# Performance work log

Measured on AMD Instinct MI355X. Metric: run time of the kernel, lower is better.

Reference implementation:

```python
import jax, jax.numpy as jnp
import numpy as np
from jax import lax

D_MODEL = 512
D_INNER = 1024   # expand=2
D_STATE = 16
D_CONV = 4
DT_RANK = 32     # ceil(d_model/16)
D_FFN = 2048
EPS = 1e-6


def _layernorm(x, g, b):
    mu = jnp.mean(x, axis=-1, keepdims=True)
    var = jnp.mean((x - mu) ** 2, axis=-1, keepdims=True)
    return (x - mu) * lax.rsqrt(var + EPS) * g + b


def _mamba(x, in_w, conv_w, conv_b, xproj_w, dt_w, dt_b, A_log, D_vec, out_w):
    # x: [B, L, d_model]
    B, L, _ = x.shape
    xz = jnp.einsum('bld,ed->ble', x, in_w)           # [B, L, 2*d_inner]
    xc, z = xz[..., :D_INNER], xz[..., D_INNER:]
    # causal depthwise conv over time
    xt = xc.transpose(0, 2, 1)                        # [B, d_inner, L]
    kern = conv_w[:, None, :]                         # [d_inner, 1, d_conv]
    xt = lax.conv_general_dilated(xt, kern, (1,), [(D_CONV - 1, 0)],
                                  feature_group_count=D_INNER)
    xc = jax.nn.silu(xt.transpose(0, 2, 1) + conv_b)  # [B, L, d_inner]
    # input-dependent SSM parameters
    x_dbl = jnp.einsum('bld,ed->ble', xc, xproj_w)    # [B, L, dt_rank+2*d_state]
    dt = x_dbl[..., :DT_RANK]
    Bm = x_dbl[..., DT_RANK:DT_RANK + D_STATE]
    Cm = x_dbl[..., DT_RANK + D_STATE:]
    delta = jax.nn.softplus(jnp.einsum('blr,dr->bld', dt, dt_w) + dt_b)  # [B, L, d_inner]
    A = -jnp.exp(A_log)                               # [d_inner, d_state]

    def step(h, inp):
        d_t, u_t, b_t, c_t = inp                      # [B,di],[B,di],[B,ds],[B,ds]
        dA = jnp.exp(d_t[:, :, None] * A)             # [B, di, ds]
        dBu = (d_t * u_t)[:, :, None] * b_t[:, None, :]
        h = dA * h + dBu
        y = jnp.einsum('bds,bs->bd', h, c_t)
        return h, y

    h0 = jnp.zeros((B, D_INNER, D_STATE), x.dtype)
    xs = (delta.transpose(1, 0, 2), xc.transpose(1, 0, 2),
          Bm.transpose(1, 0, 2), Cm.transpose(1, 0, 2))
    _, ys = lax.scan(step, h0, xs)                    # [L, B, d_inner]
    y = ys.transpose(1, 0, 2) + xc * D_vec
    y = y * jax.nn.silu(z)
    return jnp.einsum('ble,de->bld', y, out_w)        # [B, L, d_model]


def setup_inputs() -> dict:
    key = jax.random.key(0)
    ks = iter(jax.random.split(key, 40))
    B, S, T = 8, 512, 1024

    def nrm(shape, scale=0.02):
        return jax.random.normal(next(ks), shape, dtype=jnp.float32) * scale

    def mamba_params(prefix):
        A_log = jnp.log(jnp.broadcast_to(jnp.arange(1, D_STATE + 1, dtype=jnp.float32),
                                         (D_INNER, D_STATE)))
        return {
            prefix + '_in_w': nrm((2 * D_INNER, D_MODEL)),
            prefix + '_conv_w': nrm((D_INNER, D_CONV), 0.1),
            prefix + '_conv_b': jnp.zeros((D_INNER,), jnp.float32),
            prefix + '_xproj_w': nrm((DT_RANK + 2 * D_STATE, D_INNER)),
            prefix + '_dt_w': nrm((D_INNER, DT_RANK), 0.1),
            prefix + '_dt_b': jnp.full((D_INNER,), -4.0, jnp.float32),
            prefix + '_A_log': A_log,
            prefix + '_D_vec': jnp.ones((D_INNER,), jnp.float32),
            prefix + '_out_w': nrm((D_MODEL, D_INNER)),
        }

    inp = {
        'tgt': jax.random.normal(next(ks), (B, S, D_MODEL), dtype=jnp.float32),
        'memory': jax.random.normal(next(ks), (B, T, D_MODEL), dtype=jnp.float32),
    }
    inp.update(mamba_params('self'))
    inp.update(mamba_params('cross'))
    inp.update({
        'ln1_g': jnp.ones((D_MODEL,), jnp.float32), 'ln1_b': jnp.zeros((D_MODEL,), jnp.float32),
        'ln2_g': jnp.ones((D_MODEL,), jnp.float32), 'ln2_b': jnp.zeros((D_MODEL,), jnp.float32),
        'ln3_g': jnp.ones((D_MODEL,), jnp.float32), 'ln3_b': jnp.zeros((D_MODEL,), jnp.float32),
        'ffn_w1': nrm((D_FFN, D_MODEL)), 'ffn_b1': jnp.zeros((D_FFN,), jnp.float32),
        'ffn_w2': nrm((D_MODEL, D_FFN)), 'ffn_b2': jnp.zeros((D_MODEL,), jnp.float32),
    })
    return inp


def reference(tgt, memory,
              self_in_w, self_conv_w, self_conv_b, self_xproj_w, self_dt_w, self_dt_b,
              self_A_log, self_D_vec, self_out_w,
              cross_in_w, cross_conv_w, cross_conv_b, cross_xproj_w, cross_dt_w, cross_dt_b,
              cross_A_log, cross_D_vec, cross_out_w,
              ln1_g, ln1_b, ln2_g, ln2_b, ln3_g, ln3_b,
              ffn_w1, ffn_b1, ffn_w2, ffn_b2):
    S = tgt.shape[1]
    # self-Mamba block (post-norm, dropout=0)
    t2 = _mamba(tgt, self_in_w, self_conv_w, self_conv_b, self_xproj_w,
                self_dt_w, self_dt_b, self_A_log, self_D_vec, self_out_w)
    t = _layernorm(tgt + t2, ln1_g, ln1_b)
    # cross-Mamba: scan over [memory; tgt], keep last S steps
    cat = jnp.concatenate([memory, t], axis=1)
    c2 = _mamba(cat, cross_in_w, cross_conv_w, cross_conv_b, cross_xproj_w,
                cross_dt_w, cross_dt_b, cross_A_log, cross_D_vec, cross_out_w)[:, -S:]
    t = _layernorm(t + c2, ln2_g, ln2_b)
    # positionwise FFN
    f = jnp.einsum('bld,fd->blf', t, ffn_w1) + ffn_b1
    f = jax.nn.relu(f)
    f = jnp.einsum('blf,df->bld', f, ffn_w2) + ffn_b2
    t = _layernorm(t + f, ln3_g, ln3_b)
    return t
```

## Files before the change

kernel.cpp:

```cpp
#include <hip/hip_runtime.h>
#include <math.h>

#define DM    512
#define DI    1024
#define DSN   16
#define DTR   32
#define DFFN  2048
#define BB    8
#define SS    512
#define TTM   1024
#define LCAT  1536
#define NC    64
#define CONV_R 8

#define ACT_NONE     0
#define ACT_RELU     1
#define ACT_DELTA    3
#define ACT_XDBL     4

typedef __attribute__((ext_vector_type(8))) short short8;
typedef __attribute__((ext_vector_type(8))) unsigned short ushort8;
typedef __attribute__((ext_vector_type(4))) float f32x4;

#define L2E 1.4426950408889634f

__device__ __forceinline__ unsigned short f2b(float f) {
    unsigned int u = __float_as_uint(f);
    return (unsigned short)((u + 0x7FFFu + ((u >> 16) & 1u)) >> 16);
}
__device__ __forceinline__ float b2f(unsigned short h) {
    return __uint_as_float(((unsigned int)h) << 16);
}
__device__ __forceinline__ float fast_softplus(float v) {
    return (v > 20.f) ? v : __logf(1.f + __expf(v));
}
__device__ __forceinline__ float fexp2(float x) {
#if __has_builtin(__builtin_amdgcn_exp2f)
    return __builtin_amdgcn_exp2f(x);
#else
    float r; asm("v_exp_f32 %0, %1" : "=v"(r) : "v"(x)); return r;
#endif
}
__device__ __forceinline__ float frcp(float x) {
    return __builtin_amdgcn_rcpf(x);
}
__device__ __forceinline__ void gld16(const void* g, void* l) {
    __builtin_amdgcn_global_load_lds(
        (const __attribute__((address_space(1))) void*)g,
        (__attribute__((address_space(3))) void*)l, 16, 0, 0);
}

__device__ __forceinline__ int map_row(int m, int mb, int bs, int ro) {
    int q = m / mb;
    return q * bs + ro + (m - q * mb);
}

__global__ __launch_bounds__(256) void mgemm_kernel(
    const unsigned short* __restrict__ A, int mb, int bs, int ro,
    const unsigned short* __restrict__ W, const float* __restrict__ bias,
    float* __restrict__ Cf, unsigned short* __restrict__ Cb,
    float* __restrict__ C2, float* __restrict__ Cf2,
    int N, int K, int act,
    int omb, int obs, int oro, int ldc, int nofs)
{
    __shared__ __align__(16) unsigned short As[128 * 64];
    __shared__ __align__(16) unsigned short Bs[128 * 64];
    int tid = threadIdx.x;
    int lane = tid & 63, wave = tid >> 6;
    int wy = wave >> 1, wx = wave & 1;
    int nx = gridDim.x;
    int f = blockIdx.y * nx + blockIdx.x;
    int xcd = f & 7, j2 = f >> 3;
    int bandh = gridDim.y >> 3;
    int m0 = (xcd * bandh + j2 / nx) * 128;
    int n0 = (j2 % nx) * 128;
    int Kh = K / gridDim.z;
    int kbeg = blockIdx.z * Kh, kend = kbeg + Kh;
    float* Cfo = Cf;
    const float* biaso = bias;
    if (blockIdx.z) { Cfo = Cf2; biaso = nullptr; }

    const unsigned short* ga[4];
    const unsigned short* gb[4];
    unsigned short* la[4];
    unsigned short* lb[4];
    #pragma unroll
    for (int j = 0; j < 4; j++) {
        int c  = wave * 256 + j * 64 + lane;
        int r  = c >> 3;
        int q  = c & 7;
        int g  = (q & 4) | ((q & 3) ^ (r & 3));
        int arow = map_row(m0 + r, mb, bs, ro);
        ga[j] = A + (size_t)arow * K + g * 8;
        gb[j] = W + (size_t)(n0 + r) * K + g * 8;
        la[j] = As + (size_t)(wave * 256 + j * 64) * 8;
        lb[j] = Bs + (size_t)(wave * 256 + j * 64) * 8;
    }
    int fm = lane & 15, fg = lane >> 4;
    int sw = fg ^ (fm & 3);
    const unsigned short* arp = As + ((size_t)(wy * 64 + fm) * 8 + sw) * 8;
    const unsigned short* brp = Bs + ((size_t)(wx * 64 + fm) * 8 + sw) * 8;

    f32x4 acc[4][4];
    #pragma unroll
    for (int i = 0; i < 4; i++)
        #pragma unroll
        for (int j = 0; j < 4; j++) acc[i][j] = 0.f;

    for (int k0 = kbeg; k0 < kend; k0 += 64) {
        #pragma unroll
        for (int j = 0; j < 4; j++) {
            gld16(ga[j] + k0, la[j]);
            gld16(gb[j] + k0, lb[j]);
        }
        __syncthreads();
        #pragma unroll
        for (int h = 0; h < 2; h++) {
            short8 af[4], bfr[4];
            #pragma unroll
            for (int t = 0; t < 4; t++) af[t]  = *(const short8*)(arp + h * 32 + t * 1024);
            #pragma unroll
            for (int t = 0; t < 4; t++) bfr[t] = *(const short8*)(brp + h * 32 + t * 1024);
            #pragma unroll
            for (int i = 0; i < 4; i++)
                #pragma unroll
                for (int j = 0; j < 4; j++)
                    acc[i][j] = __builtin_amdgcn_mfma_f32_16x16x32_bf16(af[i], bfr[j], acc[i][j], 0, 0, 0);
        }
        __syncthreads();
    }

    int en = lane & 15, em = (lane >> 4) * 4;
    if (act == ACT_XDBL) {
        #pragma unroll
        for (int j = 0; j < 4; j++) {
            int n = n0 + wx * 64 + j * 16 + en;
            if (n >= 64) continue;
            #pragma unroll
            for (int i = 0; i < 4; i++) {
                int mbase = m0 + wy * 64 + i * 16 + em;
                #pragma unroll
                for (int r = 0; r < 4; r++) {
                    float v = acc[i][j][r];
                    int m = mbase + r;
                    if (n < 32) {
                        Cb[(size_t)m * 64 + n] = f2b(v);
                    } else {
                        C2[(size_t)m * 32 + (n - 32)] = v;
                        Cb[(size_t)m * 64 + n] = 0;
                    }
                }
            }
        }
        return;
    }
    if (act == ACT_DELTA) {
        #pragma unroll
        for (int j = 0; j < 4; j++) {
            int n = n0 + wx * 64 + j * 16 + en;
            float bv = bias[n];
            #pragma unroll
            for (int i = 0; i < 4; i++) {
                int mbase = m0 + wy * 64 + i * 16 + em;
                #pragma unroll
                for (int r = 0; r < 4; r++) {
                    float v = acc[i][j][r] + bv;
                    Cb[(size_t)(mbase + r) * 1024 + n] = f2b(fast_softplus(v));
                }
            }
        }
        return;
    }
    #pragma unroll
    for (int j = 0; j < 4; j++) {
        int n = n0 + wx * 64 + j * 16 + en;
        float bv = biaso ? biaso[n] : 0.f;
        #pragma unroll
        for (int i = 0; i < 4; i++) {
            int mbase = m0 + wy * 64 + i * 16 + em;
            #pragma unroll
            for (int r = 0; r < 4; r++) {
                float v = acc[i][j][r] + bv;
                if (act == ACT_RELU) v = v > 0.f ? v : 0.f;
                int orow = map_row(mbase + r, omb, obs, oro);
                size_t off = (size_t)orow * ldc + nofs + n;
                if (Cb) Cb[off] = f2b(v);
                else    Cfo[off] = v;
            }
        }
    }
}

__global__ void xprojb_fill(const float* __restrict__ xproj, unsigned short* __restrict__ out)
{
    int idx = blockIdx.x * 256 + threadIdx.x;
    if (idx >= 131072) return;
    int n = idx >> 10;
    out[idx] = (n < 64) ? f2b(xproj[idx]) : (unsigned short)0;
}
__global__ void dtwb_fill(const float* __restrict__ dt_w, unsigned short* __restrict__ out)
{
    int idx = blockIdx.x * 256 + threadIdx.x;
    if (idx >= 65536) return;
    int n = idx >> 6, c = idx & 63;
    out[idx] = (c < 32) ? f2b(dt_w[n * 32 + c]) : (unsigned short)0;
}

__global__ __launch_bounds__(256) void conv_silu_kernel(
    const unsigned short* __restrict__ xz,
    const float* __restrict__ cw,
    const float* __restrict__ cb,
    unsigned short* __restrict__ xc, int L, int total)
{
    int idx = blockIdx.x * blockDim.x + threadIdx.x;
    if (idx >= total) return;
    int d8 = idx & 127;
    int d0 = d8 * 8;
    int t  = idx >> 7;
    int nq = L / CONV_R;
    int b  = t / nq;
    int l0 = (t - b * nq) * CONV_R;
    size_t rbase = (size_t)b * L + l0;

    float4 wv[8];
    #pragma unroll
    for (int j = 0; j < 8; j++) wv[j] = *(const float4*)(cw + (d0 + j) * 4);
    float bias[8];
    {
        float4 c0 = ((const float4*)(cb + d0))[0];
        float4 c1 = ((const float4*)(cb + d0))[1];
        bias[0]=c0.x; bias[1]=c0.y; bias[2]=c0.z; bias[3]=c0.w;
        bias[4]=c1.x; bias[5]=c1.y; bias[6]=c1.z; bias[7]=c1.w;
    }
    ushort8 win[CONV_R + 3];
    #pragma unroll
    for (int k = 0; k < 3; k++) {
        ushort8 z;
        #pragma unroll
        for (int j = 0; j < 8; j++) z[j] = 0;
        win[k] = (l0 - 3 + k >= 0)
            ? *(const ushort8*)(xz + (rbase - 3 + k) * 2048 + d0) : z;
    }
    #pragma unroll
    for (int i = 0; i < CONV_R; i++)
        win[3 + i] = *(const ushort8*)(xz + (rbase + i) * 2048 + d0);

    const float* w = (const float*)&wv[0];
    #pragma unroll
    for (int i = 0; i < CONV_R; i++) {
        float acc[8];
        #pragma unroll
        for (int j = 0; j < 8; j++) acc[j] = bias[j];
        #pragma unroll
        for (int k = 0; k < 4; k++) {
            ushort8 v = win[i + k];
            #pragma unroll
            for (int j = 0; j < 8; j++)
                acc[j] = fmaf(b2f(v[j]), w[j * 4 + k], acc[j]);
        }
        ushort8 o;
        #pragma unroll
        for (int j = 0; j < 8; j++)
            o[j] = f2b(acc[j] * frcp(1.f + __expf(-acc[j])));
        *(ushort8*)(xc + (rbase + i) * 1024 + d0) = o;
    }
}

__global__ __launch_bounds__(256) void scan_part1(
    const unsigned short* __restrict__ delta, const unsigned short* __restrict__ xc,
    const float* __restrict__ bc, const float* __restrict__ A_log,
    float* __restrict__ part_h, float* __restrict__ part_s, int L, int CH)
{
    int tid = threadIdx.x;
    int dblk = blockIdx.x & 3;
    int c    = (blockIdx.x >> 2) & (NC - 1);
    int b    = blockIdx.x / (4 * NC);
    int d    = dblk * 256 + tid;
    float A2[DSN];
    {
        const float4* ap = (const float4*)(A_log + d * DSN);
        #pragma unroll
        for (int q = 0; q < 4; q++) {
            float4 a4 = ap[q];
            A2[q*4+0] = -__expf(a4.x) * L2E;
            A2[q*4+1] = -__expf(a4.y) * L2E;
            A2[q*4+2] = -__expf(a4.z) * L2E;
            A2[q*4+3] = -__expf(a4.w) * L2E;
        }
    }
    float h[DSN];
    #pragma unroll
    for (int s = 0; s < DSN; s++) h[s] = 0.f;
    float ssum = 0.f;
    int l0 = c * CH;
    for (int l = l0; l < l0 + CH; l++) {
        size_t r = (size_t)b * L + l;
        float4 bq[4];
        const float4* bp = (const float4*)(bc + r * 32);
        #pragma unroll
        for (int q = 0; q < 4; q++) bq[q] = bp[q];
        const float* Bm = (const float*)&bq[0];
        float dl = b2f(delta[r * DI + d]);
        float u  = b2f(xc[r * DI + d]);
        float du = dl * u;
        ssum += dl;
        #pragma unroll
        for (int s = 0; s < DSN; s++)
            h[s] = fmaf(fexp2(dl * A2[s]), h[s], du * Bm[s]);
    }
    size_t base = ((size_t)(b * NC + c) * DI + d) * DSN;
    #pragma unroll
    for (int q = 0; q < 4; q++)
        ((float4*)(part_h + base))[q] = make_float4(h[q*4], h[q*4+1], h[q*4+2], h[q*4+3]);
    part_s[(size_t)(b * NC + c) * DI + d] = ssum;
}

__global__ __launch_bounds__(256) void scan_combine(
    const float* __restrict__ A_log,
    float* __restrict__ part_h, const float* __restrict__ part_s)
{
    int idx = blockIdx.x * 256 + threadIdx.x;
    int s  = idx & (DSN - 1);
    int dd = (idx >> 4) & (DI - 1);
    int b  = idx >> 14;
    float A2 = -__expf(A_log[dd * DSN + s]) * L2E;
    float h = 0.f;
    size_t sbase = (size_t)b * NC * DI + dd;
    size_t hbase = ((size_t)b * NC * DI + dd) * DSN + s;
    for (int c = 0; c < NC; c++) {
        float ph = part_h[hbase];
        float S  = part_s[sbase];
        part_h[hbase] = h;
        h = fmaf(fexp2(A2 * S), h, ph);
        hbase += (size_t)DI * DSN;
        sbase += DI;
    }
}

__global__ __launch_bounds__(256) void scan_part2(
    const unsigned short* __restrict__ delta, const unsigned short* __restrict__ xc,
    const float* __restrict__ bc, const unsigned short* __restrict__ xz,
    const float* __restrict__ A_log, const float* __restrict__ Dv,
    const float* __restrict__ part_h,
    unsigned short* __restrict__ out, int L, int CH, int c0, int lmin)
{
    int tid = threadIdx.x;
    int dblk = blockIdx.x & 3;
    int rest = blockIdx.x >> 2;
    int ncp  = NC - c0;
    int c    = c0 + rest % ncp;
    int b    = rest / ncp;
    int d    = dblk * 256 + tid;
    float A2[DSN];
    {
        const float4* ap = (const float4*)(A_log + d * DSN);
        #pragma unroll
        for (int q = 0; q < 4; q++) {
            float4 a4 = ap[q];
            A2[q*4+0] = -__expf(a4.x) * L2E;
            A2[q*4+1] = -__expf(a4.y) * L2E;
            A2[q*4+2] = -__expf(a4.z) * L2E;
            A2[q*4+3] = -__expf(a4.w) * L2E;
        }
    }
    float Dvd = Dv[d];
    size_t base = ((size_t)(b * NC + c) * DI + d) * DSN;
    float h4[4][4];
    #pragma unroll
    for (int q = 0; q < 4; q++) *((float4*)h4[q]) = ((const float4*)(part_h + base))[q];
    float h[DSN];
    #pragma unroll
    for (int s = 0; s < DSN; s++) h[s] = h4[s >> 2][s & 3];
    int l0 = c * CH;
    for (int l = l0; l < l0 + CH; l++) {
        size_t r = (size_t)b * L + l;
        float4 bq[8];
        const float4* bp = (const float4*)(bc + r * 32);
        #pragma unroll
        for (int q = 0; q < 8; q++) bq[q] = bp[q];
        const float* Bm = (const float*)&bq[0];
        const float* Cm = Bm + DSN;
        float dl = b2f(delta[r * DI + d]);
        float u  = b2f(xc[r * DI + d]);
        float du = dl * u;
        float y = 0.f;
        #pragma unroll
        for (int s = 0; s < DSN; s++) {
            h[s] = fmaf(fexp2(dl * A2[s]), h[s], du * Bm[s]);
            y = fmaf(h[s], Cm[s], y);
        }
        if (l >= lmin) {
            float z = b2f(xz[r * 2048 + DI + d]);
            float sil = z * frcp(1.f + __expf(-z));
            out[r * DI + d] = f2b((y + u * Dvd) * sil);
        }
    }
}

__global__ __launch_bounds__(128) void addln_kernel(
    const float* __restrict__ a, int amb, int absd, int aro, int lda,
    const float* __restrict__ bsrc, const float* __restrict__ bsrc2,
    const float* __restrict__ g, const float* __restrict__ be,
    float* __restrict__ outf, int omb, int obsd, int oro, int ldo,
    unsigned short* __restrict__ outb, int bmb, int bbsd, int bro, int ldb)
{
    int m = blockIdx.x, t = threadIdx.x;
    int ar = map_row(m, amb, absd, aro);
    float4 x4 = ((const float4*)(a + (size_t)ar * lda))[t];
    float4 y4 = ((const float4*)(bsrc + (size_t)m * DM))[t];
    float v[4] = {x4.x + y4.x, x4.y + y4.y, x4.z + y4.z, x4.w + y4.w};
    if (bsrc2) {
        float4 z4 = ((const float4*)(bsrc2 + (size_t)m * DM))[t];
        v[0] += z4.x; v[1] += z4.y; v[2] += z4.z; v[3] += z4.w;
    }
    float sum = v[0] + v[1] + v[2] + v[3];
    float sq  = v[0]*v[0] + v[1]*v[1] + v[2]*v[2] + v[3]*v[3];
    #pragma unroll
    for (int o = 32; o > 0; o >>= 1) {
        sum += __shfl_down(sum, o);
        sq  += __shfl_down(sq, o);
    }
    __shared__ float s0[2], s1[2];
    if ((t & 63) == 0) { s0[t >> 6] = sum; s1[t >> 6] = sq; }
    __syncthreads();
    float tot = s0[0] + s0[1];
    float tsq = s1[0] + s1[1];
    float mu = tot * (1.f / DM);
    float var = tsq * (1.f / DM) - mu * mu;
    float rs = rsqrtf(var + 1e-6f);
    float4 g4 = ((const float4*)g)[t];
    float4 b4 = ((const float4*)be)[t];
    float o0 = (v[0] - mu) * rs * g4.x + b4.x;
    float o1 = (v[1] - mu) * rs * g4.y + b4.y;
    float o2 = (v[2] - mu) * rs * g4.z + b4.z;
    float o3 = (v[3] - mu) * rs * g4.w + b4.w;
    if (outf) {
        int orow = map_row(m, omb, obsd, oro);
        ((float4*)(outf + (size_t)orow * ldo))[t] = make_float4(o0, o1, o2, o3);
    }
    if (outb) {
        int brow = map_row(m, bmb, bbsd, bro);
        ((ushort4*)(outb + (size_t)brow * ldb))[t] =
            make_ushort4(f2b(o0), f2b(o1), f2b(o2), f2b(o3));
    }
}

__global__ void f2b_kernel(const float* __restrict__ in, unsigned short* __restrict__ out, int n4)
{
    int i = blockIdx.x * 256 + threadIdx.x;
    if (i >= n4) return;
    float4 v = ((const float4*)in)[i];
    ((ushort4*)out)[i] = make_ushort4(f2b(v.x), f2b(v.y), f2b(v.z), f2b(v.w));
}

struct W6 { const float* p[6]; };
__global__ void wconv_kernel(W6 w, unsigned short* __restrict__ out)
{
    const int cum[7] = {0, 262144, 524288, 655360, 786432, 1048576, 1310720};
    int i = blockIdx.x * 256 + threadIdx.x;
    if (i >= 1310720) return;
    int seg = 0;
    #pragma unroll
    for (int s = 1; s < 6; s++) seg += (i >= cum[s]);
    float4 v = ((const float4*)w.p[seg])[i - cum[seg]];
    ((ushort4*)out)[i] = make_ushort4(f2b(v.x), f2b(v.y), f2b(v.z), f2b(v.w));
}

__global__ void mem2catb_kernel(const float* __restrict__ mem, unsigned short* __restrict__ catb)
{
    int f = blockIdx.x * blockDim.x + threadIdx.x;
    const int total = BB * TTM * DM / 4;
    if (f >= total) return;
    const int per_b = TTM * DM / 4;
    int b = f / per_b, rem = f - b * per_b;
    float4 v = ((const float4*)mem)[f];
    ((ushort4*)catb)[(size_t)b * (LCAT * DM / 4) + rem] =
        make_ushort4(f2b(v.x), f2b(v.y), f2b(v.z), f2b(v.w));
}

static void run_scan(const unsigned short* dltb, const unsigned short* xcb, const float* bc,
                     const unsigned short* xzb, const float* A_log, const float* Dv,
                     float* part_h, float* part_s, unsigned short* out, int L,
                     int c0, int lmin, hipStream_t stream)
{
    int CH = L / NC;
    int blocks1 = BB * NC * (DI / 256);
    scan_part1<<<blocks1, 256, 0, stream>>>(dltb, xcb, bc, A_log, part_h, part_s, L, CH);
    scan_combine<<<BB * DI * DSN / 256, 256, 0, stream>>>(A_log, part_h, part_s);
    int blocks2 = BB * (NC - c0) * (DI / 256);
    scan_part2<<<blocks2, 256, 0, stream>>>(dltb, xcb, bc, xzb, A_log, Dv, part_h, out, L, CH, c0, lmin);
}

extern "C" void kernel_launch(void* const* d_in, const int* in_sizes, int n_in,
                              void* d_out, int out_size, void* d_ws, size_t ws_size,
                              hipStream_t stream)
{
    const float* tgt       = (const float*)d_in[0];
    const float* memory    = (const float*)d_in[1];
    const float* s_in_w    = (const float*)d_in[2];
    const float* s_conv_w  = (const float*)d_in[3];
    const float* s_conv_b  = (const float*)d_in[4];
    const float* s_xproj_w = (const float*)d_in[5];
    const float* s_dt_w    = (const float*)d_in[6];
    const float* s_dt_b    = (const float*)d_in[7];
    const float* s_A_log   = (const float*)d_in[8];
    const float* s_D_vec   = (const float*)d_in[9];
    const float* s_out_w   = (const float*)d_in[10];
    const float* c_in_w    = (const float*)d_in[11];
    const float* c_conv_w  = (const float*)d_in[12];
    const float* c_conv_b  = (const float*)d_in[13];
    const float* c_xproj_w = (const float*)d_in[14];
    const float* c_dt_w    = (const float*)d_in[15];
    const float* c_dt_b    = (const float*)d_in[16];
    const float* c_A_log   = (const float*)d_in[17];
    const float* c_D_vec   = (const float*)d_in[18];
    const float* c_out_w   = (const float*)d_in[19];
    const float* ln1_g     = (const float*)d_in[20];
    const float* ln1_b     = (const float*)d_in[21];
    const float* ln2_g     = (const float*)d_in[22];
    const float* ln2_b     = (const float*)d_in[23];
    const float* ln3_g     = (const float*)d_in[24];
    const float* ln3_b     = (const float*)d_in[25];
    const float* ffn_w1    = (const float*)d_in[26];
    const float* ffn_b1    = (const float*)d_in[27];
    const float* ffn_w2    = (const float*)d_in[28];
    const float* ffn_b2    = (const float*)d_in[29];
    float* outp = (float*)d_out;

    float* ws     = (float*)d_ws;
    float* bc     = ws;
    float* t1     = bc     + 393216;
    float* tbuf   = t1     + 2097152;
    float* part_h = tbuf   + 2097152;
    float* proj   = part_h;
    float* proj2  = part_h + 2097152;
    float* part_s = part_h + 8388608;
    unsigned short* ub      = (unsigned short*)(part_s + 524288);
    unsigned short* dltb    = ub;
    unsigned short* catb    = dltb    + 12582912;
    unsigned short* tgtb    = catb    + 6291456;
    unsigned short* xzb     = tgtb    + 2097152;
    unsigned short* xcb     = xzb     + 25165824;
    unsigned short* ygb     = xcb     + 12582912;
    unsigned short* tbbf    = ygb     + 12582912;
    unsigned short* s_in_wb = tbbf    + 2097152;
    unsigned short* c_in_wb = s_in_wb + 1048576;
    unsigned short* s_out_wb= c_in_wb + 1048576;
    unsigned short* c_out_wb= s_out_wb+ 524288;
    unsigned short* w1b     = c_out_wb+ 524288;
    unsigned short* w2b     = w1b     + 1048576;
    unsigned short* xprojb_s= w2b     + 1048576;
    unsigned short* xprojb_c= xprojb_s+ 131072;
    unsigned short* dtwb_s  = xprojb_c+ 131072;
    unsigned short* dtwb_c  = dtwb_s  + 65536;
    unsigned short* dtb     = dtwb_c  + 65536;
    unsigned short* fbuf    = xzb;
    float* ffnout  = (float*)dltb;
    float* ffnout2 = ffnout + 2097152;

    f2b_kernel<<<(2097152/4 + 255)/256, 256, 0, stream>>>(tgt, tgtb, 2097152/4);
    mem2catb_kernel<<<(BB*TTM*DM/4 + 255)/256, 256, 0, stream>>>(memory, catb);
    {
        W6 w; w.p[0]=s_in_w; w.p[1]=c_in_w; w.p[2]=s_out_w; w.p[3]=c_out_w; w.p[4]=ffn_w1; w.p[5]=ffn_w2;
        wconv_kernel<<<(1310720 + 255)/256, 256, 0, stream>>>(w, s_in_wb);
    }
    xprojb_fill<<<131072/256, 256, 0, stream>>>(s_xproj_w, xprojb_s);
    xprojb_fill<<<131072/256, 256, 0, stream>>>(c_xproj_w, xprojb_c);
    dtwb_fill<<<65536/256, 256, 0, stream>>>(s_dt_w, dtwb_s);
    dtwb_fill<<<65536/256, 256, 0, stream>>>(c_dt_w, dtwb_c);

    mgemm_kernel<<<dim3(2048/128, 4096/128), 256, 0, stream>>>(
        tgtb, 4096, 0, 0, s_in_wb, nullptr, nullptr, xzb, nullptr, nullptr, 2048, 512, ACT_NONE,
        4096, 0, 0, 2048, 0);
    conv_silu_kernel<<<(BB*(SS/CONV_R)*128 + 255)/256, 256, 0, stream>>>(
        xzb, s_conv_w, s_conv_b, xcb, SS, BB*(SS/CONV_R)*128);
    mgemm_kernel<<<dim3(1, 4096/128), 256, 0, stream>>>(
        xcb, 4096, 0, 0, xprojb_s, nullptr, nullptr, dtb, bc, nullptr, 128, 1024, ACT_XDBL,
        4096, 0, 0, 128, 0);
    mgemm_kernel<<<dim3(1024/128, 4096/128), 256, 0, stream>>>(
        dtb, 4096, 0, 0, dtwb_s, s_dt_b, nullptr, dltb, nullptr, nullptr, 1024, 64, ACT_DELTA,
        4096, 0, 0, 1024, 0);
    run_scan(dltb, xcb, bc, xzb, s_A_log, s_D_vec, part_h, part_s, ygb, SS, 0, 0, stream);
    mgemm_kernel<<<dim3(512/128, 4096/128, 2), 256, 0, stream>>>(
        ygb, 4096, 0, 0, s_out_wb, nullptr, proj, nullptr, nullptr, proj2, 512, 1024, ACT_NONE,
        4096, 0, 0, 512, 0);
    addln_kernel<<<4096, 128, 0, stream>>>(
        tgt, 4096, 0, 0, DM, proj, proj2, ln1_g, ln1_b,
        t1, 4096, 0, 0, DM, catb, 512, 1536, 1024, DM);

    mgemm_kernel<<<dim3(1024/128, 12288/128), 256, 0, stream>>>(
        catb, 12288, 0, 0, c_in_wb, nullptr, nullptr, xzb, nullptr, nullptr, 2048, 512, ACT_NONE,
        12288, 0, 0, 2048, 0);
    mgemm_kernel<<<dim3(1024/128, 4096/128), 256, 0, stream>>>(
        catb, 512, 1536, 1024, c_in_wb + 1024 * 512, nullptr, nullptr, xzb, nullptr, nullptr, 2048, 512, ACT_NONE,
        512, 1536, 1024, 2048, 1024);
    conv_silu_kernel<<<(BB*(LCAT/CONV_R)*128 + 255)/256, 256, 0, stream>>>(
        xzb, c_conv_w, c_conv_b, xcb, LCAT, BB*(LCAT/CONV_R)*128);
    mgemm_kernel<<<dim3(1, 12288/128), 256, 0, stream>>>(
        xcb, 12288, 0, 0, xprojb_c, nullptr, nullptr, dtb, bc, nullptr, 128, 1024, ACT_XDBL,
        12288, 0, 0, 128, 0);
    mgemm_kernel<<<dim3(1024/128, 12288/128), 256, 0, stream>>>(
        dtb, 12288, 0, 0, dtwb_c, c_dt_b, nullptr, dltb, nullptr, nullptr, 1024, 64, ACT_DELTA,
        12288, 0, 0, 1024, 0);
    run_scan(dltb, xcb, bc, xzb, c_A_log, c_D_vec, part_h, part_s, ygb, LCAT, 42, 1024, stream);
    mgemm_kernel<<<dim3(512/128, 4096/128, 2), 256, 0, stream>>>(
        ygb, 512, 1536, 1024, c_out_wb, nullptr, proj, nullptr, nullptr, proj2, 512, 1024, ACT_NONE,
        4096, 0, 0, 512, 0);
    addln_kernel<<<4096, 128, 0, stream>>>(
        t1, 4096, 0, 0, DM, proj, proj2, ln2_g, ln2_b,
        tbuf, 4096, 0, 0, DM, tbbf, 4096, 0, 0, DM);

    mgemm_kernel<<<dim3(2048/128, 4096/128), 256, 0, stream>>>(
        tbbf, 4096, 0, 0, w1b, ffn_b1, nullptr, fbuf, nullptr, nullptr, 2048, 512, ACT_RELU,
        4096, 0, 0, 2048, 0);
    mgemm_kernel<<<dim3(512/128, 4096/128, 2), 256, 0, stream>>>(
        fbuf, 4096, 0, 0, w2b, ffn_b2, ffnout, nullptr, nullptr, ffnout2, 512, 2048, ACT_NONE,
        4096, 0, 0, 512, 0);
    addln_kernel<<<4096, 128, 0, stream>>>(
        tbuf, 4096, 0, 0, DM, ffnout, ffnout2, ln3_g, ln3_b,
        outp, 4096, 0, 0, DM, nullptr, 0, 0, 0, 0);
}
```

Before: 530.5 us.

## Split-K x_proj GEMM with combine kernel, widen LDS swizzle, fuse prep kernels

The narrow x_proj GEMM (N=128, grid of 32 or 96 blocks) now uses a 4-way K split. Partial fp32 results go to a scratch buffer, and a new xdbl_combine kernel sums them and writes the bf16 dt and fp32 B/C outputs. This gives more blocks to fill the GPU. The LDS swizzle is widened from 2 to 3 bits, with a matching half-offset flip on reads, to reduce bank conflicts. The seven input and weight conversion launches are merged into one prep_kernel to cut launch overhead. In exchange, the split adds an extra kernel launch and a round trip of partial sums through memory.

Result: faster. 495.9 us (-6.5%).

```diff
diff --git a/kernel.cpp b/kernel.cpp
--- a/kernel.cpp
+++ b/kernel.cpp
@@ -89,7 +89,7 @@
         int c  = wave * 256 + j * 64 + lane;
         int r  = c >> 3;
         int q  = c & 7;
-        int g  = (q & 4) | ((q & 3) ^ (r & 3));
+        int g  = q ^ (r & 7);
         int arow = map_row(m0 + r, mb, bs, ro);
         ga[j] = A + (size_t)arow * K + g * 8;
         gb[j] = W + (size_t)(n0 + r) * K + g * 8;
@@ -98,6 +98,7 @@
     }
     int fm = lane & 15, fg = lane >> 4;
     int sw = fg ^ (fm & 3);
+    int b2 = (fm >> 2) & 1;
     const unsigned short* arp = As + ((size_t)(wy * 64 + fm) * 8 + sw) * 8;
     const unsigned short* brp = Bs + ((size_t)(wx * 64 + fm) * 8 + sw) * 8;
 
@@ -116,11 +117,12 @@
         __syncthreads();
         #pragma unroll
         for (int h = 0; h < 2; h++) {
+            int ho = ((h ^ b2) * 32);
             short8 af[4], bfr[4];
             #pragma unroll
-            for (int t = 0; t < 4; t++) af[t]  = *(const short8*)(arp + h * 32 + t * 1024);
+            for (int t = 0; t < 4; t++) af[t]  = *(const short8*)(arp + ho + t * 1024);
             #pragma unroll
-            for (int t = 0; t < 4; t++) bfr[t] = *(const short8*)(brp + h * 32 + t * 1024);
+            for (int t = 0; t < 4; t++) bfr[t] = *(const short8*)(brp + ho + t * 1024);
             #pragma unroll
             for (int i = 0; i < 4; i++)
                 #pragma unroll
@@ -132,6 +134,7 @@
 
     int en = lane & 15, em = (lane >> 4) * 4;
     if (act == ACT_XDBL) {
+        size_t zb = (size_t)blockIdx.z * omb;
         #pragma unroll
         for (int j = 0; j < 4; j++) {
             int n = n0 + wx * 64 + j * 16 + en;
@@ -140,16 +143,8 @@
             for (int i = 0; i < 4; i++) {
                 int mbase = m0 + wy * 64 + i * 16 + em;
                 #pragma unroll
-                for (int r = 0; r < 4; r++) {
-                    float v = acc[i][j][r];
-                    int m = mbase + r;
-                    if (n < 32) {
-                        Cb[(size_t)m * 64 + n] = f2b(v);
-                    } else {
-                        C2[(size_t)m * 32 + (n - 32)] = v;
-                        Cb[(size_t)m * 64 + n] = 0;
-                    }
-                }
+                for (int r = 0; r < 4; r++)
+                    C2[(zb + mbase + r) * 64 + n] = acc[i][j][r];
             }
         }
         return;
@@ -191,19 +186,89 @@
     }
 }
 
-__global__ void xprojb_fill(const float* __restrict__ xproj, unsigned short* __restrict__ out)
+__global__ __launch_bounds__(256) void xdbl_combine(
+    const float* __restrict__ pxd, unsigned short* __restrict__ dtb,
+    float* __restrict__ bcout, int M, int Z)
 {
     int idx = blockIdx.x * 256 + threadIdx.x;
-    if (idx >= 131072) return;
-    int n = idx >> 10;
-    out[idx] = (n < 64) ? f2b(xproj[idx]) : (unsigned short)0;
-}
-__global__ void dtwb_fill(const float* __restrict__ dt_w, unsigned short* __restrict__ out)
-{
-    int idx = blockIdx.x * 256 + threadIdx.x;
-    if (idx >= 65536) return;
-    int n = idx >> 6, c = idx & 63;
-    out[idx] = (c < 32) ? f2b(dt_w[n * 32 + c]) : (unsigned short)0;
+    int m = idx >> 4, n4 = idx & 15;
+    int n = n4 * 4;
+    float4 s = make_float4(0.f, 0.f, 0.f, 0.f);
+    for (int z = 0; z < Z; z++) {
+        float4 p = *(const float4*)(pxd + ((size_t)z * M + m) * 64 + n);
+        s.x += p.x; s.y += p.y; s.z += p.z; s.w += p.w;
+    }
+    if (n < 32) {
+        ((ushort4*)(dtb + (size_t)m * 64))[n4] =
+            make_ushort4(f2b(s.x), f2b(s.y), f2b(s.z), f2b(s.w));
+    } else {
+        *(float4*)(bcout + (size_t)m * 32 + (n - 32)) = s;
+        ((ushort4*)(dtb + (size_t)m * 64))[n4] = make_ushort4(0, 0, 0, 0);
+    }
+}
+
+struct PrepPtrs {
+    const float* tgt; const float* mem;
+    const float* w[6];
+    const float* xpj_s; const float* xpj_c;
+    const float* dtw_s; const float* dtw_c;
+    unsigned short* tgtb; unsigned short* catb; unsigned short* wb;
+    unsigned short* xprojb_s; unsigned short* xprojb_c;
+    unsigned short* dtwb_s; unsigned short* dtwb_c;
+};
+__global__ __launch_bounds__(256) void prep_kernel(PrepPtrs p)
+{
+    int u = blockIdx.x * 256 + threadIdx.x;
+    if (u < 524288) {
+        float4 v = ((const float4*)p.tgt)[u];
+        ((ushort4*)p.tgtb)[u] = make_ushort4(f2b(v.x), f2b(v.y), f2b(v.z), f2b(v.w));
+        return;
+    }
+    if (u < 1572864) {
+        int f = u - 524288;
+        int b = f >> 17, rem = f & 131071;
+        float4 v = ((const float4*)p.mem)[f];
+        ((ushort4*)p.catb)[(size_t)b * 196608 + rem] =
+            make_ushort4(f2b(v.x), f2b(v.y), f2b(v.z), f2b(v.w));
+        return;
+    }
+    if (u < 2883584) {
+        const int cum[7] = {0, 262144, 524288, 655360, 786432, 1048576, 1310720};
+        int i = u - 1572864;
+        int seg = 0;
+        #pragma unroll
+        for (int s = 1; s < 6; s++) seg += (i >= cum[s]);
+        float4 v = ((const float4*)p.w[seg])[i - cum[seg]];
+        ((ushort4*)p.wb)[i] = make_ushort4(f2b(v.x), f2b(v.y), f2b(v.z), f2b(v.w));
+        return;
+    }
+    if (u < 2949120) {
+        int i = u - 2883584;
+        const float* src = p.xpj_s;
+        unsigned short* dst = p.xprojb_s;
+        if (i >= 32768) { i -= 32768; src = p.xpj_c; dst = p.xprojb_c; }
+        int n = i >> 8;
+        ushort4 o = make_ushort4(0, 0, 0, 0);
+        if (n < 64) {
+            float4 v = ((const float4*)src)[i];
+            o = make_ushort4(f2b(v.x), f2b(v.y), f2b(v.z), f2b(v.w));
+        }
+        ((ushort4*)dst)[i] = o;
+        return;
+    }
+    {
+        int i = u - 2949120;
+        const float* src = p.dtw_s;
+        unsigned short* dst = p.dtwb_s;
+        if (i >= 16384) { i -= 16384; src = p.dtw_c; dst = p.dtwb_c; }
+        int n = i >> 4, c = (i & 15) * 4;
+        ushort4 o = make_ushort4(0, 0, 0, 0);
+        if (c < 32) {
+            float4 v = *(const float4*)(src + n * 32 + c);
+            o = make_ushort4(f2b(v.x), f2b(v.y), f2b(v.z), f2b(v.w));
+        }
+        ((ushort4*)dst)[i] = o;
+    }
 }
 
 __global__ __launch_bounds__(256) void conv_silu_kernel(
@@ -443,39 +508,6 @@
         ((ushort4*)(outb + (size_t)brow * ldb))[t] =
             make_ushort4(f2b(o0), f2b(o1), f2b(o2), f2b(o3));
     }
-}
-
-__global__ void f2b_kernel(const float* __restrict__ in, unsigned short* __restrict__ out, int n4)
-{
-    int i = blockIdx.x * 256 + threadIdx.x;
-    if (i >= n4) return;
-    float4 v = ((const float4*)in)[i];
-    ((ushort4*)out)[i] = make_ushort4(f2b(v.x), f2b(v.y), f2b(v.z), f2b(v.w));
-}
-
-struct W6 { const float* p[6]; };
-__global__ void wconv_kernel(W6 w, unsigned short* __restrict__ out)
-{
-    const int cum[7] = {0, 262144, 524288, 655360, 786432, 1048576, 1310720};
-    int i = blockIdx.x * 256 + threadIdx.x;
-    if (i >= 1310720) return;
-    int seg = 0;
-    #pragma unroll
-    for (int s = 1; s < 6; s++) seg += (i >= cum[s]);
-    float4 v = ((const float4*)w.p[seg])[i - cum[seg]];
-    ((ushort4*)out)[i] = make_ushort4(f2b(v.x), f2b(v.y), f2b(v.z), f2b(v.w));
-}
-
-__global__ void mem2catb_kernel(const float* __restrict__ mem, unsigned short* __restrict__ catb)
-{
-    int f = blockIdx.x * blockDim.x + threadIdx.x;
-    const int total = BB * TTM * DM / 4;
-    if (f >= total) return;
-    const int per_b = TTM * DM / 4;
-    int b = f / per_b, rem = f - b * per_b;
-    float4 v = ((const float4*)mem)[f];
-    ((ushort4*)catb)[(size_t)b * (LCAT * DM / 4) + rem] =
-        make_ushort4(f2b(v.x), f2b(v.y), f2b(v.z), f2b(v.w));
 }
 
 static void run_scan(const unsigned short* dltb, const unsigned short* xcb, const float* bc,
@@ -534,6 +566,7 @@
     float* part_h = tbuf   + 2097152;
     float* proj   = part_h;
     float* proj2  = part_h + 2097152;
+    float* pxd    = part_h;
     float* part_s = part_h + 8388608;
     unsigned short* ub      = (unsigned short*)(part_s + 524288);
     unsigned short* dltb    = ub;
@@ -558,25 +591,27 @@
     float* ffnout  = (float*)dltb;
     float* ffnout2 = ffnout + 2097152;
 
-    f2b_kernel<<<(2097152/4 + 255)/256, 256, 0, stream>>>(tgt, tgtb, 2097152/4);
-    mem2catb_kernel<<<(BB*TTM*DM/4 + 255)/256, 256, 0, stream>>>(memory, catb);
     {
-        W6 w; w.p[0]=s_in_w; w.p[1]=c_in_w; w.p[2]=s_out_w; w.p[3]=c_out_w; w.p[4]=ffn_w1; w.p[5]=ffn_w2;
-        wconv_kernel<<<(1310720 + 255)/256, 256, 0, stream>>>(w, s_in_wb);
-    }
-    xprojb_fill<<<131072/256, 256, 0, stream>>>(s_xproj_w, xprojb_s);
-    xprojb_fill<<<131072/256, 256, 0, stream>>>(c_xproj_w, xprojb_c);
-    dtwb_fill<<<65536/256, 256, 0, stream>>>(s_dt_w, dtwb_s);
-    dtwb_fill<<<65536/256, 256, 0, stream>>>(c_dt_w, dtwb_c);
+        PrepPtrs pp;
+        pp.tgt = tgt; pp.mem = memory;
+        pp.w[0]=s_in_w; pp.w[1]=c_in_w; pp.w[2]=s_out_w; pp.w[3]=c_out_w; pp.w[4]=ffn_w1; pp.w[5]=ffn_w2;
+        pp.xpj_s = s_xproj_w; pp.xpj_c = c_xproj_w;
+        pp.dtw_s = s_dt_w;    pp.dtw_c = c_dt_w;
+        pp.tgtb = tgtb; pp.catb = catb; pp.wb = s_in_wb;
+        pp.xprojb_s = xprojb_s; pp.xprojb_c = xprojb_c;
+        pp.dtwb_s = dtwb_s; pp.dtwb_c = dtwb_c;
+        prep_kernel<<<11648, 256, 0, stream>>>(pp);
+    }
 
     mgemm_kernel<<<dim3(2048/128, 4096/128), 256, 0, stream>>>(
         tgtb, 4096, 0, 0, s_in_wb, nullptr, nullptr, xzb, nullptr, nullptr, 2048, 512, ACT_NONE,
         4096, 0, 0, 2048, 0);
     conv_silu_kernel<<<(BB*(SS/CONV_R)*128 + 255)/256, 256, 0, stream>>>(
         xzb, s_conv_w, s_conv_b, xcb, SS, BB*(SS/CONV_R)*128);
-    mgemm_kernel<<<dim3(1, 4096/128), 256, 0, stream>>>(
-        xcb, 4096, 0, 0, xprojb_s, nullptr, nullptr, dtb, bc, nullptr, 128, 1024, ACT_XDBL,
-        4096, 0, 0, 128, 0);
+    mgemm_kernel<<<dim3(1, 4096/128, 4), 256, 0, stream>>>(
+        xcb, 4096, 0, 0, xprojb_s, nullptr, nullptr, nullptr, pxd, nullptr, 128, 1024, ACT_XDBL,
+        4096, 0, 0, 0, 0);
+    xdbl_combine<<<4096*16/256, 256, 0, stream>>>(pxd, dtb, bc, 4096, 4);
     mgemm_kernel<<<dim3(1024/128, 4096/128), 256, 0, stream>>>(
         dtb, 4096, 0, 0, dtwb_s, s_dt_b, nullptr, dltb, nullptr, nullptr, 1024, 64, ACT_DELTA,
         4096, 0, 0, 1024, 0);
@@ -596,9 +631,10 @@
         512, 1536, 1024, 2048, 1024);
     conv_silu_kernel<<<(BB*(LCAT/CONV_R)*128 + 255)/256, 256, 0, stream>>>(
         xzb, c_conv_w, c_conv_b, xcb, LCAT, BB*(LCAT/CONV_R)*128);
-    mgemm_kernel<<<dim3(1, 12288/128), 256, 0, stream>>>(
-        xcb, 12288, 0, 0, xprojb_c, nullptr, nullptr, dtb, bc, nullptr, 128, 1024, ACT_XDBL,
-        12288, 0, 0, 128, 0);
+    mgemm_kernel<<<dim3(1, 12288/128, 4), 256, 0, stream>>>(
+        xcb, 12288, 0, 0, xprojb_c, nullptr, nullptr, nullptr, pxd, nullptr, 128, 1024, ACT_XDBL,
+        12288, 0, 0, 0, 0);
+    xdbl_combine<<<12288*16/256, 256, 0, stream>>>(pxd, dtb, bc, 12288, 4);
     mgemm_kernel<<<dim3(1024/128, 12288/128), 256, 0, stream>>>(
         dtb, 12288, 0, 0, dtwb_c, c_dt_b, nullptr, dltb, nullptr, nullptr, 1024, 64, ACT_DELTA,
         12288, 0, 0, 1024, 0);
```
